# Optimization experiments

Hardware: AMD Instinct MI355X
Metric: run time of the kernel (lower is better)

The kernel has to match this reference:

```python
import jax, jax.numpy as jnp
import numpy as np

NUM_GROUPS = 8
NUM_HEADS = 4
EPS = 1e-5


def group_norm(x, w, b):
    # x: [B, C, H, W]; normalize over (C/G, H, W) within each of G groups
    B, C, H, W = x.shape
    xg = x.reshape(B, NUM_GROUPS, C // NUM_GROUPS, H, W)
    mean = xg.mean(axis=(2, 3, 4), keepdims=True)
    var = xg.var(axis=(2, 3, 4), keepdims=True)
    xn = ((xg - mean) * jax.lax.rsqrt(var + EPS)).reshape(B, C, H, W)
    return xn * w[None, :, None, None] + b[None, :, None, None]


def setup_inputs() -> dict:
    key = jax.random.key(0)
    ks = jax.random.split(key, 7)
    B, C, H, W = 4, 256, 64, 64
    x = jax.random.normal(ks[0], (B, C, H, W), dtype=jnp.float32)
    gn_w = jax.random.normal(ks[1], (C,), dtype=jnp.float32) * 0.1 + 1.0
    gn_b = jax.random.normal(ks[2], (C,), dtype=jnp.float32) * 0.1
    qkv_w = jax.random.normal(ks[3], (3 * C, C), dtype=jnp.float32) / np.sqrt(C)
    qkv_b = jax.random.normal(ks[4], (3 * C,), dtype=jnp.float32) * 0.02
    proj_w = jax.random.normal(ks[5], (C, C), dtype=jnp.float32) / np.sqrt(C)
    proj_b = jax.random.normal(ks[6], (C,), dtype=jnp.float32) * 0.02
    return {"x": x, "gn_w": gn_w, "gn_b": gn_b, "qkv_w": qkv_w,
            "qkv_b": qkv_b, "proj_w": proj_w, "proj_b": proj_b}


def reference(x, gn_w, gn_b, qkv_w, qkv_b, proj_w, proj_b):
    B, C, H, W = x.shape
    nh = NUM_HEADS
    hd = C // nh
    scale = hd ** -0.5
    N = H * W

    h = group_norm(x, gn_w, gn_b)
    # 1x1 conv == channel matmul: [B, 3C, H, W]
    qkv = jnp.einsum('oc,bchw->bohw', qkv_w, h) + qkv_b[None, :, None, None]
    qkv = qkv.reshape(B, 3, nh, hd, N)  # matches torch .view(B,3,nh,hd,HW)
    q, k, v = qkv[:, 0], qkv[:, 1], qkv[:, 2]  # each [B, nh, hd, N]

    attn = jnp.einsum('bhdn,bhdm->bhnm', q, k) * scale  # [B, nh, N, N]
    attn = jax.nn.softmax(attn, axis=-1)
    out = jnp.einsum('bhnm,bhdm->bhdn', attn, v)  # [B, nh, hd, N]
    out = out.reshape(B, C, H, W)

    proj = jnp.einsum('oc,bchw->bohw', proj_w, out) + proj_b[None, :, None, None]
    return x + proj
```

## Files before the change

### kernel.cpp

```cpp
#include <hip/hip_runtime.h>
#include <hip/hip_bf16.h>

#define BB   4
#define CC   256
#define NN   4096
#define NH   4
#define HD   64
#define NG   8
#define GSZ  32
#define EPSV 1e-5f
#define SCALE_L2E 0.18033688f

typedef __bf16 bf16x8 __attribute__((ext_vector_type(8)));
typedef float  f32x4  __attribute__((ext_vector_type(4)));

#define MFMA16(a, b, c)  __builtin_amdgcn_mfma_f32_16x16x32_bf16((a), (b), (c), 0, 0, 0)

#if __has_builtin(__builtin_amdgcn_exp2f)
#define EXP2F __builtin_amdgcn_exp2f
#else
#define EXP2F exp2f
#endif

#define WAITV(n)  asm volatile("s_waitcnt vmcnt(" #n ")" ::: "memory")
#define WAITL0    asm volatile("s_waitcnt lgkmcnt(0)" ::: "memory")
#define SBAR      __builtin_amdgcn_s_barrier()
#define SCHED0    __builtin_amdgcn_sched_barrier(0)

__device__ inline unsigned short f2bf(float f) {
    unsigned int u = __float_as_uint(f);
    u += 0x7fffu + ((u >> 16) & 1u);
    return (unsigned short)(u >> 16);
}

__device__ __forceinline__ bf16x8 pk8(const f32x4& p0, const f32x4& p1) {
    alignas(16) unsigned int u[4];
    u[0] = __builtin_amdgcn_perm(__float_as_uint(p0[1]), __float_as_uint(p0[0]), 0x07060302u);
    u[1] = __builtin_amdgcn_perm(__float_as_uint(p0[3]), __float_as_uint(p0[2]), 0x07060302u);
    u[2] = __builtin_amdgcn_perm(__float_as_uint(p1[1]), __float_as_uint(p1[0]), 0x07060302u);
    u[3] = __builtin_amdgcn_perm(__float_as_uint(p1[3]), __float_as_uint(p1[2]), 0x07060302u);
    return *reinterpret_cast<bf16x8*>(u);
}

__device__ __forceinline__ void async_ld16(void* lds, const void* g) {
    __builtin_amdgcn_global_load_lds(
        (const __attribute__((address_space(1))) unsigned int*)g,
        (__attribute__((address_space(3))) unsigned int*)lds, 16, 0, 0);
}

__global__ void k_prep(const float* __restrict__ x, float* __restrict__ stats,
                       const float* __restrict__ wp, unsigned short* __restrict__ op) {
    int blk = blockIdx.x;
    int t = threadIdx.x;
    if (blk >= 256) {
        int i = (blk - 256) * 256 + t;
        if (i < CC * CC) op[i] = f2bf(wp[i]);
        return;
    }
    int b = blk >> 6, g = (blk >> 3) & 7, s = blk & 7;
    const float* p = x + ((size_t)(b * CC + g * GSZ)) * NN + s * 16384;
    float s0 = 0.f, s1 = 0.f;
    #pragma unroll
    for (int i = 0; i < 64; ++i) { float v = p[i * 256 + t]; s0 += v; s1 += v * v; }
    #pragma unroll
    for (int m = 1; m <= 32; m <<= 1) { s0 += __shfl_xor(s0, m); s1 += __shfl_xor(s1, m); }
    __shared__ float ls[8];
    int w = t >> 6;
    if ((t & 63) == 0) { ls[w * 2] = s0; ls[w * 2 + 1] = s1; }
    __syncthreads();
    if (t == 0) {
        float a0 = ls[0] + ls[2] + ls[4] + ls[6];
        float a1 = ls[1] + ls[3] + ls[5] + ls[7];
        stats[((b * NG + g) * 8 + s) * 2 + 0] = a0;
        stats[((b * NG + g) * 8 + s) * 2 + 1] = a1;
    }
}

__global__ void __launch_bounds__(256)
k_tab(const float* __restrict__ wq, const float* __restrict__ gw, const float* __restrict__ gb,
      const float* __restrict__ qb, const float* __restrict__ stats,
      unsigned short* __restrict__ wqp, float* __restrict__ biasq) {
    int o = blockIdx.x, c = threadIdx.x;
    int g = c >> 5;
    float w = wq[o * CC + c];
    float gwc = gw[c], gbc = gb[c];
    __shared__ float ls[4][4];
    #pragma unroll
    for (int b = 0; b < 4; ++b) {
        float s0 = 0.f, s1 = 0.f;
        #pragma unroll
        for (int s = 0; s < 8; ++s) {
            s0 += stats[((b * NG + g) * 8 + s) * 2 + 0];
            s1 += stats[((b * NG + g) * 8 + s) * 2 + 1];
        }
        float mean = s0 * (1.0f / 131072.0f);
        float var  = s1 * (1.0f / 131072.0f) - mean * mean;
        float inv  = rsqrtf(var + EPSV);
        float Ac = gwc * inv;
        float Bc = gbc - mean * Ac;
        wqp[((size_t)b * 768 + o) * CC + c] = f2bf(w * Ac);
        float p = w * Bc;
        #pragma unroll
        for (int m = 1; m <= 32; m <<= 1) p += __shfl_xor(p, m);
        if ((c & 63) == 0) ls[b][c >> 6] = p;
    }
    __syncthreads();
    if (c < 4) biasq[c * 768 + o] = qb[o] + ls[c][0] + ls[c][1] + ls[c][2] + ls[c][3];
}

__global__ void __launch_bounds__(256)
k_qkv(const float* __restrict__ x, const unsigned short* __restrict__ wqp,
      const float* __restrict__ biasq,
      unsigned short* __restrict__ qt, unsigned short* __restrict__ kt,
      unsigned short* __restrict__ vt) {
    int bx = blockIdx.x, by = blockIdx.y;
    int t = threadIdx.x, wave = t >> 6, lane = t & 63;
    int l15 = lane & 15, quad = lane >> 4;
    int wm = wave >> 1, wn = wave & 1;

    __shared__ alignas(16) unsigned char smem[49152];

    int nn0 = bx * 128;
    int b = nn0 >> 12, nbase = nn0 & 4095;

    const char* Ag = (const char*)wqp + (size_t)b * 393216 + (size_t)by * 65536;
    int row0 = t >> 2, slot = t & 3;
    size_t a0 = (size_t)row0 * 512 + slot * 16;
    size_t a1 = a0 + 64 * 512;
    unsigned int dstA = wave * 1024;

    int colsrc = (((lane & 31) * 16) - 32 * wave) & 511;
    const char* xrow = (const char*)x +
        (((size_t)(b * CC) + (wave * 8 + (lane >> 5))) * NN + nbase) * 4 + colsrc;

    auto stage = [&](int buf, int kk) {
        async_ld16(smem + buf * 8192 + dstA,        Ag + a0 + (size_t)kk * 64);
        async_ld16(smem + buf * 8192 + 4096 + dstA, Ag + a1 + (size_t)kk * 64);
        const char* bs = xrow + (size_t)kk * 32 * NN * 4;
        unsigned char* bd = smem + 16384 + buf * 16384 + wave * 4096;
        async_ld16(bd,        bs);
        async_ld16(bd + 1024, bs + (size_t)2 * NN * 4);
        async_ld16(bd + 2048, bs + (size_t)4 * NN * 4);
        async_ld16(bd + 3072, bs + (size_t)6 * NN * 4);
    };

    int colr[4];
    #pragma unroll
    for (int f = 0; f < 4; ++f)
        colr[f] = (((wn * 64 + f * 16 + l15) * 4) + quad * 32) & 511;

    f32x4 acc[4][4];
    #pragma unroll
    for (int i = 0; i < 4; ++i)
        #pragma unroll
        for (int j = 0; j < 4; ++j) acc[i][j] = (f32x4){0.f, 0.f, 0.f, 0.f};

    stage(0, 0);
    stage(1, 1);

    for (int kk = 0; kk < 8; ++kk) {
        if (kk < 7) { WAITV(6); } else { WAITV(0); }
        SCHED0;
        SBAR;
        SCHED0;
        int cur = kk & 1;
        bf16x8 af[4], bf[4];
        #pragma unroll
        for (int f = 0; f < 4; ++f)
            af[f] = *reinterpret_cast<const bf16x8*>(smem + cur * 8192 + (wm * 64 + f * 16 + l15) * 64 + quad * 16);
        #pragma unroll
        for (int f = 0; f < 4; ++f) {
            const unsigned char* fb = smem + 16384 + cur * 16384 + quad * 4096 + colr[f];
            alignas(16) unsigned int u[4];
            #pragma unroll
            for (int jj = 0; jj < 4; ++jj) {
                float xl = *reinterpret_cast<const float*>(fb + (2 * jj) * 512);
                float xh = *reinterpret_cast<const float*>(fb + (2 * jj + 1) * 512);
                asm("v_cvt_pk_bf16_f32 %0, %1, %2" : "=v"(u[jj]) : "v"(xl), "v"(xh));
            }
            bf[f] = *reinterpret_cast<const bf16x8*>(u);
        }
        #pragma unroll
        for (int fm = 0; fm < 4; ++fm)
            #pragma unroll
            for (int fn = 0; fn < 4; ++fn)
                acc[fm][fn] = MFMA16(af[fm], bf[fn], acc[fm][fn]);
        WAITL0;
        SCHED0;
        SBAR;
        SCHED0;
        if (kk < 6) stage(cur, kk + 2);
    }

    int s = by >> 1;
    if (s < 2) {
        #pragma unroll
        for (int fm = 0; fm < 4; ++fm) {
            int o = by * 128 + wm * 64 + fm * 16 + quad * 4;
            int h = (o >> 6) & 3, d0 = o & 63;
            float bias[4];
            #pragma unroll
            for (int r = 0; r < 4; ++r) bias[r] = biasq[b * 768 + o + r];
            #pragma unroll
            for (int fn = 0; fn < 4; ++fn) {
                int n = nbase + wn * 64 + fn * 16 + l15;
                alignas(8) unsigned short o4[4];
                if (s == 0) {
                    #pragma unroll
                    for (int r = 0; r < 4; ++r) o4[r] = f2bf((acc[fm][fn][r] + bias[r]) * SCALE_L2E);
                    *reinterpret_cast<uint2*>(qt + (((size_t)(b * NH + h) * NN) + n) * HD + d0) =
                        *reinterpret_cast<const uint2*>(o4);
                } else {
                    #pragma unroll
                    for (int r = 0; r < 4; ++r) o4[r] = f2bf(acc[fm][fn][r] + bias[r]);
                    *reinterpret_cast<uint2*>(kt + (((size_t)(b * NH + h) * NN) + n) * HD + d0) =
                        *reinterpret_cast<const uint2*>(o4);
                }
            }
        }
    } else {
        unsigned short* vtile = (unsigned short*)smem;
        #pragma unroll
        for (int fm = 0; fm < 4; ++fm) {
            int o  = by * 128 + wm * 64 + fm * 16 + quad * 4;
            int ol = wm * 64 + fm * 16 + quad * 4;
            float bias[4];
            #pragma unroll
            for (int r = 0; r < 4; ++r) bias[r] = biasq[b * 768 + o + r];
            #pragma unroll
            for (int fn = 0; fn < 4; ++fn) {
                int nl = wn * 64 + fn * 16 + l15;
                #pragma unroll
                for (int r = 0; r < 4; ++r)
                    vtile[(ol + r) * 132 + nl] = f2bf(acc[fm][fn][r] + bias[r]);
            }
        }
        __syncthreads();
        int hbase = (by - 4) * 2;
        #pragma unroll
        for (int pass = 0; pass < 8; ++pass) {
            int row  = pass * 16 + (t >> 4);
            int col0 = (t & 15) * 8;
            int nb = (col0 & ~31) | ((col0 & 16) >> 1) | ((col0 & 8) >> 1);
            const unsigned short* src = vtile + row * 132 + nb;
            uint2 lo = *reinterpret_cast<const uint2*>(src);
            uint2 hi = *reinterpret_cast<const uint2*>(src + 16);
            uint4 o4 = make_uint4(lo.x, lo.y, hi.x, hi.y);
            int h = hbase + (row >> 6), d = row & 63;
            *reinterpret_cast<uint4*>(vt + ((size_t)(b * NH + h) * HD + d) * NN + nbase + col0) = o4;
        }
    }
}

__global__ void __launch_bounds__(256, 4)
k_attn(const unsigned short* __restrict__ qt, const unsigned short* __restrict__ kt,
       const unsigned short* __restrict__ vt, unsigned short* __restrict__ ao) {
    int lid = blockIdx.x;
    int xcd = lid & 7, slot = lid >> 3;
    int bh = xcd + ((slot >> 5) << 3);
    int qtile = slot & 31;
    int t = threadIdx.x, wave = t >> 6, lane = t & 63;
    int l15 = lane & 15, quad = lane >> 4;
    int qbase = qtile * 128 + wave * 32;
    const unsigned short* qp = qt + (size_t)bh * NN * HD;
    const unsigned short* kp = kt + (size_t)bh * NN * HD;
    const unsigned short* vp = vt + (size_t)bh * HD * NN;

    __shared__ alignas(16) unsigned char kbuf[2][8192];
    __shared__ alignas(16) unsigned char vbuf[2][8192];

    int lr8 = lane >> 3, lc8 = lane & 7;
    int swz = lc8 ^ lr8;
    const char* ksrc = (const char*)kp + (size_t)(wave * 16 + lr8) * 128 + swz * 16;
    const char* vsrc = (const char*)vp + (size_t)(wave * 16 + lr8) * 8192 + swz * 16;
    unsigned int dstw = wave * 2048;

    auto stage = [&](int buf) {
        async_ld16(kbuf[buf] + dstw,        ksrc);
        async_ld16(kbuf[buf] + dstw + 1024, ksrc + 1024);
        ksrc += 8192;
        async_ld16(vbuf[buf] + dstw,        vsrc);
        async_ld16(vbuf[buf] + dstw + 1024, vsrc + 8 * 8192);
        vsrc += 128;
    };

    bf16x8 qaA0 = *reinterpret_cast<const bf16x8*>(qp + (size_t)(qbase + l15) * HD + quad * 8);
    bf16x8 qaA1 = *reinterpret_cast<const bf16x8*>(qp + (size_t)(qbase + l15) * HD + 32 + quad * 8);
    bf16x8 qaB0 = *reinterpret_cast<const bf16x8*>(qp + (size_t)(qbase + 16 + l15) * HD + quad * 8);
    bf16x8 qaB1 = *reinterpret_cast<const bf16x8*>(qp + (size_t)(qbase + 16 + l15) * HD + 32 + quad * 8);

    const f32x4 Z4 = (f32x4){0.f, 0.f, 0.f, 0.f};
    bf16x8 vone;
    #pragma unroll
    for (int i = 0; i < 8; ++i) vone[i] = (__bf16)1.0f;

    f32x4 OA[4], OB[4];
    #pragma unroll
    for (int i = 0; i < 4; ++i) { OA[i] = Z4; OB[i] = Z4; }
    f32x4 liAA = Z4, liBB = Z4;

    int sx = l15 & 7;

    auto compute = [&](const unsigned char* kb, const unsigned char* vbb) {
        f32x4 sA0[2], sA1[2], sB0[2], sB1[2];
        __builtin_amdgcn_s_setprio(1);
        #pragma unroll
        for (int s = 0; s < 2; ++s) {
            int r0 = (s * 32 + l15) * 128;
            bf16x8 k00 = *reinterpret_cast<const bf16x8*>(kb + r0 + ((quad ^ sx) * 16));
            bf16x8 k01 = *reinterpret_cast<const bf16x8*>(kb + r0 + (((quad + 4) ^ sx) * 16));
            bf16x8 k10 = *reinterpret_cast<const bf16x8*>(kb + r0 + 2048 + ((quad ^ sx) * 16));
            bf16x8 k11 = *reinterpret_cast<const bf16x8*>(kb + r0 + 2048 + (((quad + 4) ^ sx) * 16));
            sA0[s] = MFMA16(k00, qaA0, Z4);  sA0[s] = MFMA16(k01, qaA1, sA0[s]);
            sA1[s] = MFMA16(k10, qaA0, Z4);  sA1[s] = MFMA16(k11, qaA1, sA1[s]);
            sB0[s] = MFMA16(k00, qaB0, Z4);  sB0[s] = MFMA16(k01, qaB1, sB0[s]);
            sB1[s] = MFMA16(k10, qaB0, Z4);  sB1[s] = MFMA16(k11, qaB1, sB1[s]);
        }
        __builtin_amdgcn_s_setprio(0);
        #pragma unroll
        for (int s = 0; s < 2; ++s) {
            f32x4 pA0, pA1, pB0, pB1;
            #pragma unroll
            for (int r = 0; r < 4; ++r) {
                pA0[r] = EXP2F(sA0[s][r]);  pA1[r] = EXP2F(sA1[s][r]);
                pB0[r] = EXP2F(sB0[s][r]);  pB1[r] = EXP2F(sB1[s][r]);
            }
            bf16x8 fA = pk8(pA0, pA1);
            bf16x8 fB = pk8(pB0, pB1);

            __builtin_amdgcn_s_setprio(1);
            liAA = MFMA16(fA, vone, liAA);
            liBB = MFMA16(fB, vone, liBB);

            #pragma unroll
            for (int dc = 0; dc < 4; ++dc) {
                const unsigned char* vrow = vbb + (dc * 16 + l15) * 128;
                bf16x8 vv = *reinterpret_cast<const bf16x8*>(vrow + (((s * 4 + quad) ^ sx) * 16));
                OA[dc] = MFMA16(fA, vv, OA[dc]);
                OB[dc] = MFMA16(fB, vv, OB[dc]);
            }
            __builtin_amdgcn_s_setprio(0);
        }
    };

    stage(0);
    __syncthreads();

    for (int p = 0; p < 32; ++p) {
        stage(1);
        compute(kbuf[0], vbuf[0]);
        __syncthreads();
        if (p < 31) stage(0);
        compute(kbuf[1], vbuf[1]);
        __syncthreads();
    }

    f32x4 rA, rB;
    #pragma unroll
    for (int r = 0; r < 4; ++r) { rA[r] = 1.0f / liAA[r]; rB[r] = 1.0f / liBB[r]; }

    int b = bh >> 2, h = bh & 3;
    #pragma unroll
    for (int dc = 0; dc < 4; ++dc) {
        #pragma unroll
        for (int r = 0; r < 4; ++r) {
            int qA = qbase + quad * 4 + r;
            ao[((size_t)(b * NN) + qA) * CC + h * HD + dc * 16 + l15]      = f2bf(OA[dc][r] * rA[r]);
            ao[((size_t)(b * NN) + qA + 16) * CC + h * HD + dc * 16 + l15] = f2bf(OB[dc][r] * rB[r]);
        }
    }
}

__global__ void __launch_bounds__(256)
k_proj(const unsigned short* __restrict__ ao, const unsigned short* __restrict__ wp,
       const float* __restrict__ pb, const float* __restrict__ x,
       float* __restrict__ out) {
    int bx = blockIdx.x, by = blockIdx.y;
    int t = threadIdx.x, wave = t >> 6, lane = t & 63;
    int l15 = lane & 15, quad = lane >> 4;
    int wm = wave >> 1, wn = wave & 1;

    __shared__ alignas(16) unsigned char At[2][4096];
    __shared__ alignas(16) unsigned char Bt[2][4096];

    const char* Ag = (const char*)wp + (size_t)by * 32768;
    const char* Bg = (const char*)ao + (size_t)bx * 32768;
    int row0 = t >> 2, slot = t & 3;
    size_t a0 = (size_t)row0 * 512 + slot * 16;
    unsigned int dst0 = wave * 1024;

    auto stage = [&](int buf, int kk) {
        size_t ko = (size_t)kk * 64;
        async_ld16(At[buf] + dst0, Ag + a0 + ko);
        async_ld16(Bt[buf] + dst0, Bg + a0 + ko);
    };

    f32x4 acc[2][2];
    #pragma unroll
    for (int i = 0; i < 2; ++i)
        #pragma unroll
        for (int j = 0; j < 2; ++j) acc[i][j] = (f32x4){0.f, 0.f, 0.f, 0.f};

    stage(0, 0);
    stage(1, 1);

    for (int kk = 0; kk < 8; ++kk) {
        if (kk < 7) { WAITV(2); } else { WAITV(0); }
        SCHED0;
        SBAR;
        SCHED0;
        int cur = kk & 1;
        bf16x8 af[2], bf[2];
        #pragma unroll
        for (int f = 0; f < 2; ++f) {
            af[f] = *reinterpret_cast<const bf16x8*>(At[cur] + (wm * 32 + f * 16 + l15) * 64 + quad * 16);
            bf[f] = *reinterpret_cast<const bf16x8*>(Bt[cur] + (wn * 32 + f * 16 + l15) * 64 + quad * 16);
        }
        #pragma unroll
        for (int fm = 0; fm < 2; ++fm)
            #pragma unroll
            for (int fn = 0; fn < 2; ++fn)
                acc[fm][fn] = MFMA16(af[fm], bf[fn], acc[fm][fn]);
        WAITL0;
        SCHED0;
        SBAR;
        SCHED0;
        if (kk < 6) stage(cur, kk + 2);
    }

    int nn0 = bx * 64;
    int b = nn0 >> 12, nbase = nn0 & 4095;
    #pragma unroll
    for (int fm = 0; fm < 2; ++fm) {
        int o = by * 64 + wm * 32 + fm * 16 + quad * 4;
        float bias[4];
        #pragma unroll
        for (int r = 0; r < 4; ++r) bias[r] = pb[o + r];
        #pragma unroll
        for (int fn = 0; fn < 2; ++fn) {
            int n = nbase + wn * 32 + fn * 16 + l15;
            #pragma unroll
            for (int r = 0; r < 4; ++r) {
                size_t idx = ((size_t)(b * CC + o + r)) * NN + n;
                out[idx] = acc[fm][fn][r] + bias[r] + x[idx];
            }
        }
    }
}

extern "C" void kernel_launch(void* const* d_in, const int* in_sizes, int n_in,
                              void* d_out, int out_size, void* d_ws, size_t ws_size,
                              hipStream_t stream) {
    const float* x     = (const float*)d_in[0];
    const float* gw    = (const float*)d_in[1];
    const float* gb    = (const float*)d_in[2];
    const float* qkvw  = (const float*)d_in[3];
    const float* qkvb  = (const float*)d_in[4];
    const float* projw = (const float*)d_in[5];
    const float* projb = (const float*)d_in[6];
    float* out = (float*)d_out;

    char* w = (char*)d_ws;
    size_t off = 0;
    unsigned short* qt = (unsigned short*)(w + off); off += (size_t)BB * NH * NN * HD * 2;
    unsigned short* kt = (unsigned short*)(w + off); off += (size_t)BB * NH * NN * HD * 2;
    unsigned short* vt = (unsigned short*)(w + off); off += (size_t)BB * NH * HD * NN * 2;
    unsigned short* ao = (unsigned short*)(w + off); off += (size_t)BB * NN * CC * 2;
    unsigned short* wqp = (unsigned short*)(w + off); off += (size_t)BB * 3 * CC * CC * 2;
    float* biasq = (float*)(w + off); off += (size_t)BB * 3 * CC * sizeof(float);
    unsigned short* wpb = (unsigned short*)(w + off); off += (size_t)CC * CC * 2;
    float* stats = (float*)(w + off); off += (size_t)BB * NG * 8 * 2 * sizeof(float);

    k_prep<<<512, 256, 0, stream>>>(x, stats, projw, wpb);
    k_tab<<<768, 256, 0, stream>>>(qkvw, gw, gb, qkvb, stats, wqp, biasq);
    k_qkv<<<dim3(BB * NN / 128, 6), 256, 0, stream>>>(x, wqp, biasq, qt, kt, vt);
    k_attn<<<512, 256, 0, stream>>>(qt, kt, vt, ao);
    k_proj<<<dim3(BB * NN / 64, CC / 64), 256, 0, stream>>>(ao, wpb, projb, x, out);
}
```

Baseline: 177.9 us.

## Split attention key range across two wave groups with LDS reduction

The attention kernel now launches 512 threads per block. Two groups of four waves each process half of the key sequence for the same query tile, with separate double-buffered K/V LDS regions (64KB total). At the end, group 1 writes its partial outputs and row sums to LDS and group 0 adds them and normalizes. This doubles the waves per query tile to raise occupancy and hide latency. In exchange it adds an LDS exchange, an extra barrier and more shared memory per block, which may cut the number of resident blocks.

```diff
diff --git a/kernel.cpp b/kernel.cpp
--- a/kernel.cpp
+++ b/kernel.cpp
@@ -252,7 +252,7 @@
     }
 }
 
-__global__ void __launch_bounds__(256, 4)
+__global__ void __launch_bounds__(512, 4)
 k_attn(const unsigned short* __restrict__ qt, const unsigned short* __restrict__ kt,
        const unsigned short* __restrict__ vt, unsigned short* __restrict__ ao) {
     int lid = blockIdx.x;
@@ -260,27 +260,30 @@
     int bh = xcd + ((slot >> 5) << 3);
     int qtile = slot & 31;
     int t = threadIdx.x, wave = t >> 6, lane = t & 63;
+    int grp = wave >> 2, wg = wave & 3;
     int l15 = lane & 15, quad = lane >> 4;
-    int qbase = qtile * 128 + wave * 32;
+    int qbase = qtile * 128 + wg * 32;
+    int kbase = grp * 2048;
     const unsigned short* qp = qt + (size_t)bh * NN * HD;
     const unsigned short* kp = kt + (size_t)bh * NN * HD;
     const unsigned short* vp = vt + (size_t)bh * HD * NN;
 
-    __shared__ alignas(16) unsigned char kbuf[2][8192];
-    __shared__ alignas(16) unsigned char vbuf[2][8192];
+    __shared__ alignas(16) unsigned char smem[65536];
 
     int lr8 = lane >> 3, lc8 = lane & 7;
     int swz = lc8 ^ lr8;
-    const char* ksrc = (const char*)kp + (size_t)(wave * 16 + lr8) * 128 + swz * 16;
-    const char* vsrc = (const char*)vp + (size_t)(wave * 16 + lr8) * 8192 + swz * 16;
-    unsigned int dstw = wave * 2048;
+    const char* ksrc = (const char*)kp + (size_t)(kbase + wg * 16 + lr8) * 128 + swz * 16;
+    const char* vsrc = (const char*)vp + (size_t)(wg * 16 + lr8) * 8192 + (size_t)kbase * 2 + swz * 16;
+    unsigned int dstw = wg * 2048;
 
     auto stage = [&](int buf) {
-        async_ld16(kbuf[buf] + dstw,        ksrc);
-        async_ld16(kbuf[buf] + dstw + 1024, ksrc + 1024);
+        unsigned char* kb = smem + grp * 16384 + buf * 8192;
+        unsigned char* vb = smem + 32768 + grp * 16384 + buf * 8192;
+        async_ld16(kb + dstw,        ksrc);
+        async_ld16(kb + dstw + 1024, ksrc + 1024);
         ksrc += 8192;
-        async_ld16(vbuf[buf] + dstw,        vsrc);
-        async_ld16(vbuf[buf] + dstw + 1024, vsrc + 8 * 8192);
+        async_ld16(vb + dstw,        vsrc);
+        async_ld16(vb + dstw + 1024, vsrc + 8 * 8192);
         vsrc += 128;
     };
 
@@ -301,7 +304,9 @@
 
     int sx = l15 & 7;
 
-    auto compute = [&](const unsigned char* kb, const unsigned char* vbb) {
+    auto compute = [&](int buf) {
+        const unsigned char* kb = smem + grp * 16384 + buf * 8192;
+        const unsigned char* vbb = smem + 32768 + grp * 16384 + buf * 8192;
         f32x4 sA0[2], sA1[2], sB0[2], sB1[2];
         __builtin_amdgcn_s_setprio(1);
         #pragma unroll
@@ -346,27 +351,53 @@
     stage(0);
     __syncthreads();
 
-    for (int p = 0; p < 32; ++p) {
+    for (int p = 0; p < 16; ++p) {
         stage(1);
-        compute(kbuf[0], vbuf[0]);
+        compute(0);
         __syncthreads();
-        if (p < 31) stage(0);
-        compute(kbuf[1], vbuf[1]);
+        if (p < 15) stage(0);
+        compute(1);
         __syncthreads();
     }
 
-    f32x4 rA, rB;
-    #pragma unroll
-    for (int r = 0; r < 4; ++r) { rA[r] = 1.0f / liAA[r]; rB[r] = 1.0f / liBB[r]; }
-
-    int b = bh >> 2, h = bh & 3;
-    #pragma unroll
-    for (int dc = 0; dc < 4; ++dc) {
-        #pragma unroll
-        for (int r = 0; r < 4; ++r) {
-            int qA = qbase + quad * 4 + r;
-            ao[((size_t)(b * NN) + qA) * CC + h * HD + dc * 16 + l15]      = f2bf(OA[dc][r] * rA[r]);
-            ao[((size_t)(b * NN) + qA + 16) * CC + h * HD + dc * 16 + l15] = f2bf(OB[dc][r] * rB[r]);
+    float* xch = (float*)smem;
+    int xi = (wg * 64 + lane) * 41;
+    if (grp == 1) {
+        #pragma unroll
+        for (int dc = 0; dc < 4; ++dc)
+            #pragma unroll
+            for (int r = 0; r < 4; ++r) {
+                xch[xi + dc * 4 + r]      = OA[dc][r];
+                xch[xi + 16 + dc * 4 + r] = OB[dc][r];
+            }
+        #pragma unroll
+        for (int r = 0; r < 4; ++r) { xch[xi + 32 + r] = liAA[r]; xch[xi + 36 + r] = liBB[r]; }
+    }
+    __syncthreads();
+    if (grp == 0) {
+        #pragma unroll
+        for (int dc = 0; dc < 4; ++dc)
+            #pragma unroll
+            for (int r = 0; r < 4; ++r) {
+                OA[dc][r] += xch[xi + dc * 4 + r];
+                OB[dc][r] += xch[xi + 16 + dc * 4 + r];
+            }
+        #pragma unroll
+        for (int r = 0; r < 4; ++r) { liAA[r] += xch[xi + 32 + r]; liBB[r] += xch[xi + 36 + r]; }
+
+        f32x4 rA, rB;
+        #pragma unroll
+        for (int r = 0; r < 4; ++r) { rA[r] = 1.0f / liAA[r]; rB[r] = 1.0f / liBB[r]; }
+
+        int b = bh >> 2, h = bh & 3;
+        #pragma unroll
+        for (int dc = 0; dc < 4; ++dc) {
+            #pragma unroll
+            for (int r = 0; r < 4; ++r) {
+                int qA = qbase + quad * 4 + r;
+                ao[((size_t)(b * NN) + qA) * CC + h * HD + dc * 16 + l15]      = f2bf(OA[dc][r] * rA[r]);
+                ao[((size_t)(b * NN) + qA + 16) * CC + h * HD + dc * 16 + l15] = f2bf(OB[dc][r] * rB[r]);
+            }
         }
     }
 }
@@ -474,6 +505,6 @@
     k_prep<<<512, 256, 0, stream>>>(x, stats, projw, wpb);
     k_tab<<<768, 256, 0, stream>>>(qkvw, gw, gb, qkvb, stats, wqp, biasq);
     k_qkv<<<dim3(BB * NN / 128, 6), 256, 0, stream>>>(x, wqp, biasq, qt, kt, vt);
-    k_attn<<<512, 256, 0, stream>>>(qt, kt, vt, ao);
+    k_attn<<<512, 512, 0, stream>>>(qt, kt, vt, ao);
     k_proj<<<dim3(BB * NN / 64, CC / 64), 256, 0, stream>>>(ao, wpb, projb, x, out);
 }
```

Measured after the change: 175.8 us. No clear change (-1.2%).
